# Optimization experiments

Hardware: AMD Instinct MI355X
Metric: run time of the kernel (lower is better)

## Reference

```python
import jax, jax.numpy as jnp
import numpy as np

BS, SEQ, D, NSLOT, NLAB = 64, 1024, 800, 64, 72  # D = 2*hidden_size
MAX_SPAN = 8

def setup_inputs() -> dict:
    key = jax.random.key(0)
    k1, k2, k3, k4 = jax.random.split(key, 4)
    batch_hs = jax.random.normal(k1, (BS, SEQ, D), dtype=jnp.float32)
    slot_begins = jax.random.randint(k2, (BS, NSLOT), 0, SEQ - MAX_SPAN, dtype=jnp.int32)
    slot_lens = jax.random.randint(k3, (BS, NSLOT), 0, MAX_SPAN, dtype=jnp.int32)
    W_clf = jax.random.normal(k4, (D, NLAB), dtype=jnp.float32) * 0.02
    b_clf = jnp.zeros((NLAB,), dtype=jnp.float32)
    return {"batch_hs": batch_hs, "slot_begins": slot_begins,
            "slot_lens": slot_lens, "W_clf": W_clf, "b_clf": b_clf}

def reference(batch_hs, slot_begins, slot_lens, W_clf, b_clf):
    # Ragged slot-range average pooling: pool_n = mean(hs[b, i_n : j_n + 1])
    # with j_n = i_n + len_n (inclusive end, as in hs[i:j+1]).
    ends = slot_begins + slot_lens                      # inclusive end index
    pos = jnp.arange(batch_hs.shape[1], dtype=slot_begins.dtype)  # (SEQ,)
    mask = (pos[None, None, :] >= slot_begins[:, :, None]) & \
           (pos[None, None, :] <= ends[:, :, None])     # (bs, n_slots, seq)
    maskf = mask.astype(batch_hs.dtype)
    counts = (slot_lens + 1).astype(batch_hs.dtype)     # span lengths
    # gather+sum over each span, then divide by span length -> mean pool
    pools = jnp.einsum('bns,bsd->bnd', maskf, batch_hs) / counts[:, :, None]
    # slot classifier (args.clf == 'clf')
    slot_logits = pools @ W_clf + b_clf                 # (bs, n_slots, n_labels)
    return slot_logits
```

## Files before the change

### kernel.cpp

```cpp
#include <hip/hip_runtime.h>


#define BS    64
#define SEQ   1024
#define DIM   800
#define NSLOT 64
#define NLAB  72
#define SPB   8
#define KTILE 160
#define NC    (DIM / 4)

__global__ __launch_bounds__(256, 2) void slot_clf_kernel(
    const float* __restrict__ hs,
    const int*   __restrict__ begins,
    const int*   __restrict__ lens,
    const float* __restrict__ W,
    const float* __restrict__ bias,
    float*       __restrict__ out)
{
    __shared__ float pool[SPB][DIM];
    __shared__ float Wt[KTILE * NLAB];
    __shared__ int s_begin[SPB];
    __shared__ int s_count[SPB];

    const int t  = threadIdx.x;
    const int b  = blockIdx.x >> 3;
    const int n0 = (blockIdx.x & 7) * SPB;

    if (t < SPB) {
        int idx = b * NSLOT + n0 + t;
        s_begin[t] = begins[idx];
        s_count[t] = lens[idx] + 1;
    }
    __syncthreads();

    for (int i = t; i < SPB * NC; i += 256) {
        int s = i / NC;
        int c = i - s * NC;
        int beg = s_begin[s];
        int cnt = s_count[s];
        const float4* rowp = (const float4*)(hs + ((size_t)b * SEQ + beg) * DIM) + c;
        float4 a0 = make_float4(0.f, 0.f, 0.f, 0.f);
        float4 a1 = make_float4(0.f, 0.f, 0.f, 0.f);
        int r = 0;
        for (; r + 2 <= cnt; r += 2) {
            float4 v0 = rowp[(size_t)r * NC];
            float4 v1 = rowp[(size_t)(r + 1) * NC];
            a0.x += v0.x; a0.y += v0.y; a0.z += v0.z; a0.w += v0.w;
            a1.x += v1.x; a1.y += v1.y; a1.z += v1.z; a1.w += v1.w;
        }
        if (r < cnt) {
            float4 v0 = rowp[(size_t)r * NC];
            a0.x += v0.x; a0.y += v0.y; a0.z += v0.z; a0.w += v0.w;
        }
        float inv = 1.0f / (float)cnt;
        pool[s][c * 4 + 0] = (a0.x + a1.x) * inv;
        pool[s][c * 4 + 1] = (a0.y + a1.y) * inv;
        pool[s][c * 4 + 2] = (a0.z + a1.z) * inv;
        pool[s][c * 4 + 3] = (a0.w + a1.w) * inv;
    }

    const int wave = t >> 6;
    const int lane = t & 63;
    const int s0   = wave * 2;
    float acc00 = 0.f, acc10 = 0.f, acc01 = 0.f, acc11 = 0.f;

    for (int k0 = 0; k0 < DIM; k0 += KTILE) {
        __syncthreads();
        const float* Wsrc = W + (size_t)k0 * NLAB;
        for (int i = t; i < KTILE * NLAB; i += 256)
            Wt[i] = Wsrc[i];
        __syncthreads();

        #pragma unroll 4
        for (int dd = 0; dd < KTILE; ++dd) {
            float p0 = pool[s0][k0 + dd];
            float p1 = pool[s0 + 1][k0 + dd];
            float w0 = Wt[dd * NLAB + lane];
            acc00 = fmaf(p0, w0, acc00);
            acc10 = fmaf(p1, w0, acc10);
            if (lane < NLAB - 64) {
                float w1 = Wt[dd * NLAB + 64 + lane];
                acc01 = fmaf(p0, w1, acc01);
                acc11 = fmaf(p1, w1, acc11);
            }
        }
    }

    float* outb = out + ((size_t)b * NSLOT + n0) * NLAB;
    outb[(s0 + 0) * NLAB + lane] = acc00 + bias[lane];
    outb[(s0 + 1) * NLAB + lane] = acc10 + bias[lane];
    if (lane < NLAB - 64) {
        outb[(s0 + 0) * NLAB + 64 + lane] = acc01 + bias[64 + lane];
        outb[(s0 + 1) * NLAB + 64 + lane] = acc11 + bias[64 + lane];
    }
}

extern "C" void kernel_launch(void* const* d_in, const int* in_sizes, int n_in,
                              void* d_out, int out_size, void* d_ws, size_t ws_size,
                              hipStream_t stream) {
    const float* hs     = (const float*)d_in[0];
    const int*   begins = (const int*)  d_in[1];
    const int*   lens   = (const int*)  d_in[2];
    const float* W      = (const float*)d_in[3];
    const float* bias   = (const float*)d_in[4];
    float*       out    = (float*)d_out;

    slot_clf_kernel<<<dim3(BS * (NSLOT / SPB)), dim3(256), 0, stream>>>(
        hs, begins, lens, W, bias, out);
}
```

Before: 311.5 us.

## Use bf16 MFMA for slot classifier with pre-transposed bf16 weights

Replaces the scalar FMA classifier loop with bf16 16x16x32 MFMA instructions. Pooled means are packed to bf16 in shared memory, zero-padded to 16 rows. A new prep kernel transposes W into a padded bf16 workspace. The block grows to 320 threads, five waves each covering 16 labels, and the shared-memory W tiling and its barriers are removed. This adds a second launch and bf16 rounding error, and the gather of hidden-state rows, likely the main cost, is unchanged.

```diff
diff --git a/kernel.cpp b/kernel.cpp
--- a/kernel.cpp
+++ b/kernel.cpp
@@ -7,19 +7,38 @@
 #define NSLOT 64
 #define NLAB  72
 #define SPB   8
-#define KTILE 160
 #define NC    (DIM / 4)
+#define PS    808
+#define NTROW 80
+#define KK    (DIM / 32)
 
-__global__ __launch_bounds__(256, 2) void slot_clf_kernel(
-    const float* __restrict__ hs,
-    const int*   __restrict__ begins,
-    const int*   __restrict__ lens,
-    const float* __restrict__ W,
-    const float* __restrict__ bias,
-    float*       __restrict__ out)
+typedef __attribute__((ext_vector_type(8))) short short8;
+typedef __attribute__((ext_vector_type(4))) float float4v;
+
+static __device__ inline unsigned short f2bf(float f) {
+    unsigned u = __builtin_bit_cast(unsigned, f);
+    u += 0x7fffu + ((u >> 16) & 1u);
+    return (unsigned short)(u >> 16);
+}
+
+__global__ void prep_wt_kernel(const float* __restrict__ W, unsigned short* __restrict__ wt) {
+    int i = blockIdx.x * 256 + threadIdx.x;
+    if (i >= NTROW * DIM) return;
+    int n = i / DIM;
+    int k = i - n * DIM;
+    float v = (n < NLAB) ? W[k * NLAB + n] : 0.0f;
+    wt[i] = f2bf(v);
+}
+
+__global__ __launch_bounds__(320, 3) void slot_clf_kernel(
+    const float*          __restrict__ hs,
+    const int*            __restrict__ begins,
+    const int*            __restrict__ lens,
+    const unsigned short* __restrict__ wt,
+    const float*          __restrict__ bias,
+    float*                __restrict__ out)
 {
-    __shared__ float pool[SPB][DIM];
-    __shared__ float Wt[KTILE * NLAB];
+    __shared__ unsigned short poolb[16 * PS];
     __shared__ int s_begin[SPB];
     __shared__ int s_count[SPB];
 
@@ -32,9 +51,13 @@
         s_begin[t] = begins[idx];
         s_count[t] = lens[idx] + 1;
     }
+    {
+        unsigned* pz = (unsigned*)(poolb + 8 * PS);
+        for (int i = t; i < 8 * PS / 2; i += 320) pz[i] = 0u;
+    }
     __syncthreads();
 
-    for (int i = t; i < SPB * NC; i += 256) {
+    for (int i = t; i < SPB * NC; i += 320) {
         int s = i / NC;
         int c = i - s * NC;
         int beg = s_begin[s];
@@ -54,45 +77,40 @@
             a0.x += v0.x; a0.y += v0.y; a0.z += v0.z; a0.w += v0.w;
         }
         float inv = 1.0f / (float)cnt;
-        pool[s][c * 4 + 0] = (a0.x + a1.x) * inv;
-        pool[s][c * 4 + 1] = (a0.y + a1.y) * inv;
-        pool[s][c * 4 + 2] = (a0.z + a1.z) * inv;
-        pool[s][c * 4 + 3] = (a0.w + a1.w) * inv;
+        ushort4 pk;
+        pk.x = f2bf((a0.x + a1.x) * inv);
+        pk.y = f2bf((a0.y + a1.y) * inv);
+        pk.z = f2bf((a0.z + a1.z) * inv);
+        pk.w = f2bf((a0.w + a1.w) * inv);
+        *(ushort4*)(poolb + s * PS + 4 * c) = pk;
     }
+    __syncthreads();
 
     const int wave = t >> 6;
     const int lane = t & 63;
-    const int s0   = wave * 2;
-    float acc00 = 0.f, acc10 = 0.f, acc01 = 0.f, acc11 = 0.f;
+    const int col  = lane & 15;
+    const int quad = lane >> 4;
 
-    for (int k0 = 0; k0 < DIM; k0 += KTILE) {
-        __syncthreads();
-        const float* Wsrc = W + (size_t)k0 * NLAB;
-        for (int i = t; i < KTILE * NLAB; i += 256)
-            Wt[i] = Wsrc[i];
-        __syncthreads();
+    const int n = wave * 16 + col;
+    const short8* ap = (const short8*)(poolb + col * PS + 8 * quad);
+    const short8* bp = (const short8*)(wt + (size_t)n * DIM + 8 * quad);
 
-        #pragma unroll 4
-        for (int dd = 0; dd < KTILE; ++dd) {
-            float p0 = pool[s0][k0 + dd];
-            float p1 = pool[s0 + 1][k0 + dd];
-            float w0 = Wt[dd * NLAB + lane];
-            acc00 = fmaf(p0, w0, acc00);
-            acc10 = fmaf(p1, w0, acc10);
-            if (lane < NLAB - 64) {
-                float w1 = Wt[dd * NLAB + 64 + lane];
-                acc01 = fmaf(p0, w1, acc01);
-                acc11 = fmaf(p1, w1, acc11);
-            }
-        }
+    float4v acc = {0.f, 0.f, 0.f, 0.f};
+    #pragma unroll 5
+    for (int kk = 0; kk < KK; ++kk) {
+        short8 a   = ap[4 * kk];
+        short8 bfr = bp[4 * kk];
+        acc = __builtin_amdgcn_mfma_f32_16x16x32_bf16(a, bfr, acc, 0, 0, 0);
     }
 
-    float* outb = out + ((size_t)b * NSLOT + n0) * NLAB;
-    outb[(s0 + 0) * NLAB + lane] = acc00 + bias[lane];
-    outb[(s0 + 1) * NLAB + lane] = acc10 + bias[lane];
-    if (lane < NLAB - 64) {
-        outb[(s0 + 0) * NLAB + 64 + lane] = acc01 + bias[64 + lane];
-        outb[(s0 + 1) * NLAB + 64 + lane] = acc11 + bias[64 + lane];
+    if (n < NLAB) {
+        float bv = bias[n];
+        float* outb = out + ((size_t)b * NSLOT + n0) * NLAB + n;
+        #pragma unroll
+        for (int r = 0; r < 4; ++r) {
+            int m = quad * 4 + r;
+            if (m < SPB) outb[(size_t)m * NLAB] = acc[r] + bv;
+        }
     }
 }
 
@@ -105,7 +123,9 @@
     const float* W      = (const float*)d_in[3];
     const float* bias   = (const float*)d_in[4];
     float*       out    = (float*)d_out;
+    unsigned short* wt  = (unsigned short*)d_ws;
 
-    slot_clf_kernel<<<dim3(BS * (NSLOT / SPB)), dim3(256), 0, stream>>>(
-        hs, begins, lens, W, bias, out);
+    prep_wt_kernel<<<dim3((NTROW * DIM + 255) / 256), dim3(256), 0, stream>>>(W, wt);
+    slot_clf_kernel<<<dim3(BS * (NSLOT / SPB)), dim3(320), 0, stream>>>(
+        hs, begins, lens, wt, bias, out);
 }
```

Result: faster. 262.9 us (-15.6%).
